# Optimization experiments

Hardware: AMD Instinct MI355X
Metric: run time of the kernel (lower is better)

The kernel has to match this reference:

```python
import jax, jax.numpy as jnp
import numpy as np

B, A, T, D = 8, 50, 256, 128
HEADS, C = 32, 4  # C = D // HEADS
NEG_SLOPE = 0.2   # PyG GATConv default negative_slope


def setup_inputs() -> dict:
    key = jax.random.key(0)
    k1, k2, k3, k4 = jax.random.split(key, 4)
    h = jax.random.normal(k1, (B, A, T, D), dtype=jnp.float32)
    # PyG Linear weight [heads*out, in], applied as x @ W.T
    W = jax.random.normal(k2, (HEADS * C, D), dtype=jnp.float32) * (1.0 / np.sqrt(D))
    att_src = jax.random.normal(k3, (HEADS, C), dtype=jnp.float32) * 0.1
    att_dst = jax.random.normal(k4, (HEADS, C), dtype=jnp.float32) * 0.1
    bias = jnp.zeros((HEADS * C,), dtype=jnp.float32)
    return {"h": h, "W": W, "att_src": att_src, "att_dst": att_dst, "bias": bias}


def reference(h, W, att_src, att_dst, bias):
    # Graph is fully-connected-minus-self over A agents, replicated B*T times.
    # Equivalent dense form: per-destination softmax over all sources j != i.
    Bv, Av, Tv, Dv = h.shape
    x = h.transpose(0, 2, 1, 3).reshape(Bv * Tv, Av, Dv)          # [N, A, D], N = B*T graphs
    x = jnp.einsum('nad,ed->nae', x, W).reshape(Bv * Tv, Av, HEADS, C)  # W x, per head
    a_src = jnp.einsum('nahc,hc->nah', x, att_src)                # alpha_src[j]
    a_dst = jnp.einsum('nahc,hc->nah', x, att_dst)                # alpha_dst[i]
    # edge (j -> i): e_ij = leaky_relu(alpha_src[j] + alpha_dst[i])
    e = a_dst[:, :, None, :] + a_src[:, None, :, :]               # [N, i, j, H]
    e = jnp.where(e > 0, e, NEG_SLOPE * e)
    diag = jnp.eye(Av, dtype=bool)[None, :, :, None]              # no self-loops
    e = jnp.where(diag, -jnp.inf, e)
    alpha = jax.nn.softmax(e, axis=2)                             # scatter-softmax over src per dst
    out = jnp.einsum('nijh,njhc->nihc', alpha, x)                 # scatter-add aggregation
    out = out.reshape(Bv * Tv, Av, HEADS * C) + bias              # concat heads + bias
    return out.reshape(Bv, Tv, Av, HEADS * C).transpose(0, 2, 1, 3)  # (B, A, T, D)
```

## Files before the change

kernel.cpp:

```cpp
#include <hip/hip_runtime.h>
#include <hip/hip_bf16.h>

#define LOG2E 1.4426950408889634f

typedef __attribute__((ext_vector_type(8))) short bf16x8;
typedef __attribute__((ext_vector_type(4))) float f32x4;
typedef __attribute__((ext_vector_type(2))) float v2f;

static __device__ __forceinline__ float fast_exp2(float x) {
    return __builtin_amdgcn_exp2f(x);
}
static __device__ __forceinline__ short bf16bits(float f) {
    __hip_bfloat16 b = __float2bfloat16(f);
    return *reinterpret_cast<short*>(&b);
}

__global__ void wconv(const float* __restrict__ W, short* __restrict__ Wb) {
    const int i = blockIdx.x * 256 + threadIdx.x;
    Wb[i] = bf16bits(W[i]);
}

template<bool PRE>
__global__ __launch_bounds__(256, 4) void gat_fused(
    const float* __restrict__ hsrc,
    const float* __restrict__ W,
    const short* __restrict__ Wb,
    const float* __restrict__ att_src,
    const float* __restrict__ att_dst,
    const float* __restrict__ bias,
    float* __restrict__ out)
{
    constexpr int A = 50, T = 256, D = 128, H = 32;
    __shared__ __align__(16) char smem[25600 + 12800];
    v2f*   EsFs = (v2f*)smem;
    v2f*   EdFd = (v2f*)(smem + 12800);
    short* hsb  = (short*)smem;
    short* xsb  = (short*)(smem + 25600);

    const int n = blockIdx.x;
    const int b = n >> 8;
    const int t = n & 255;
    const int tid = threadIdx.x;

    const float4* hg4 = (const float4*)hsrc;
    for (int idx = tid; idx < 64 * 32; idx += 256) {
        const int a = idx >> 5, k4 = idx & 31;
        short4 pk = {0, 0, 0, 0};
        if (a < A) {
            const float4 hv = hg4[((size_t)(b * A + a) * T + t) * 32 + k4];
            pk.x = bf16bits(hv.x); pk.y = bf16bits(hv.y);
            pk.z = bf16bits(hv.z); pk.w = bf16bits(hv.w);
        }
        const int swz = (k4 >> 1) ^ (a & 7);
        *(short4*)&hsb[a * 128 + swz * 8 + (k4 & 1) * 4] = pk;
    }
    __syncthreads();

    {
        const int wv = tid >> 6;
        const int lane = tid & 63;
        const int lr = lane & 15, lg = lane >> 4;
        const int n0 = wv * 32;
        f32x4 acc[4][2];
        #pragma unroll
        for (int m = 0; m < 4; ++m) {
            acc[m][0] = (f32x4){0.f, 0.f, 0.f, 0.f};
            acc[m][1] = (f32x4){0.f, 0.f, 0.f, 0.f};
        }
        #pragma unroll
        for (int kk = 0; kk < 4; ++kk) {
            bf16x8 bf0, bf1;
            if (PRE) {
                const bf16x8* Wb8 = (const bf16x8*)Wb;
                bf0 = Wb8[(size_t)(n0 + lr) * 16 + kk * 4 + lg];
                bf1 = Wb8[(size_t)(n0 + 16 + lr) * 16 + kk * 4 + lg];
            } else {
                const float4* W4 = (const float4*)W;
                const int kb = kk * 8 + lg * 2;
                const float4 wa = W4[(size_t)(n0 + lr) * 32 + kb];
                const float4 wb = W4[(size_t)(n0 + lr) * 32 + kb + 1];
                const float4 wc = W4[(size_t)(n0 + 16 + lr) * 32 + kb];
                const float4 wd = W4[(size_t)(n0 + 16 + lr) * 32 + kb + 1];
                bf0[0] = bf16bits(wa.x); bf0[1] = bf16bits(wa.y);
                bf0[2] = bf16bits(wa.z); bf0[3] = bf16bits(wa.w);
                bf0[4] = bf16bits(wb.x); bf0[5] = bf16bits(wb.y);
                bf0[6] = bf16bits(wb.z); bf0[7] = bf16bits(wb.w);
                bf1[0] = bf16bits(wc.x); bf1[1] = bf16bits(wc.y);
                bf1[2] = bf16bits(wc.z); bf1[3] = bf16bits(wc.w);
                bf1[4] = bf16bits(wd.x); bf1[5] = bf16bits(wd.y);
                bf1[6] = bf16bits(wd.z); bf1[7] = bf16bits(wd.w);
            }
            #pragma unroll
            for (int m = 0; m < 4; ++m) {
                const int row = m * 16 + lr;
                const int chunk = (kk * 4 + lg) ^ (row & 7);
                const bf16x8 af = *(const bf16x8*)&hsb[row * 128 + chunk * 8];
                acc[m][0] = __builtin_amdgcn_mfma_f32_16x16x32_bf16(af, bf0, acc[m][0], 0, 0, 0);
                acc[m][1] = __builtin_amdgcn_mfma_f32_16x16x32_bf16(af, bf1, acc[m][1], 0, 0, 0);
            }
        }
        #pragma unroll
        for (int m = 0; m < 4; ++m) {
            const int rb = m * 16 + lg * 4;
            #pragma unroll
            for (int nt = 0; nt < 2; ++nt) {
                const int col = n0 + nt * 16 + lr;
                #pragma unroll
                for (int r = 0; r < 4; ++r) {
                    if (rb + r < A) xsb[(rb + r) * D + col] = bf16bits(acc[m][nt][r]);
                }
            }
        }
    }
    __syncthreads();

    for (int idx = tid; idx < A * H; idx += 256) {
        const int hh = idx & 31, a = idx >> 5;
        const uint2 xq = *(const uint2*)&xsb[a * D + hh * 4];
        const float x0 = __uint_as_float(xq.x << 16);
        const float x1 = __uint_as_float(xq.x & 0xffff0000u);
        const float x2 = __uint_as_float(xq.y << 16);
        const float x3 = __uint_as_float(xq.y & 0xffff0000u);
        const float4 s4 = ((const float4*)att_src)[hh];
        const float4 d4 = ((const float4*)att_dst)[hh];
        const float asc = LOG2E * fmaf(x3, s4.w, fmaf(x2, s4.z, fmaf(x1, s4.y, x0 * s4.x)));
        const float ads = LOG2E * fmaf(x3, d4.w, fmaf(x2, d4.z, fmaf(x1, d4.y, x0 * d4.x)));
        EsFs[idx] = (v2f){fast_exp2(asc), fast_exp2(0.2f * asc)};
        EdFd[idx] = (v2f){fast_exp2(ads), fast_exp2(0.2f * ads)};
    }
    __syncthreads();

    {
        const int hh = tid & 31;
        const int ib = tid >> 5;
        v2f acc01[7], acc23[7], df[7];
        float l[7];
        #pragma unroll
        for (int r = 0; r < 7; ++r) {
            const int i = ib + 8 * r;
            const int ii = (i < A) ? i : (A - 1);
            df[r] = EdFd[ii * H + hh];
            acc01[r] = (v2f){0.f, 0.f};
            acc23[r] = (v2f){0.f, 0.f};
            l[r] = 0.f;
        }
        #pragma unroll 5
        for (int j = 0; j < A; ++j) {
            const v2f sf = EsFs[j * H + hh];
            const uint2 xq = *(const uint2*)&xsb[j * D + hh * 4];
            const v2f x01 = (v2f){__uint_as_float(xq.x << 16),
                                  __uint_as_float(xq.x & 0xffff0000u)};
            const v2f x23 = (v2f){__uint_as_float(xq.y << 16),
                                  __uint_as_float(xq.y & 0xffff0000u)};
            #pragma unroll
            for (int r = 0; r < 7; ++r) {
                const v2f pe = df[r] * sf;
                const float p = fmaxf(pe.x, pe.y);
                l[r] += p;
                const v2f pp = (v2f){p, p};
                acc01[r] = __builtin_elementwise_fma(pp, x01, acc01[r]);
                acc23[r] = __builtin_elementwise_fma(pp, x23, acc23[r]);
            }
        }
        const float4 bv = ((const float4*)bias)[hh];
        #pragma unroll
        for (int r = 0; r < 7; ++r) {
            const int i = ib + 8 * r;
            if (i < A) {
                const v2f sf = EsFs[i * H + hh];
                const uint2 xq = *(const uint2*)&xsb[i * D + hh * 4];
                const float xx0 = __uint_as_float(xq.x << 16);
                const float xx1 = __uint_as_float(xq.x & 0xffff0000u);
                const float xx2 = __uint_as_float(xq.y << 16);
                const float xx3 = __uint_as_float(xq.y & 0xffff0000u);
                const v2f pe = df[r] * sf;
                const float p = fmaxf(pe.x, pe.y);
                const float linv = 1.0f / (l[r] - p);
                float4 o;
                o.x = fmaf(acc01[r].x - p * xx0, linv, bv.x);
                o.y = fmaf(acc01[r].y - p * xx1, linv, bv.y);
                o.z = fmaf(acc23[r].x - p * xx2, linv, bv.z);
                o.w = fmaf(acc23[r].y - p * xx3, linv, bv.w);
                *(float4*)&out[((size_t)(b * A + i) * T + t) * D + hh * 4] = o;
            }
        }
    }
}

extern "C" void kernel_launch(void* const* d_in, const int* in_sizes, int n_in,
                              void* d_out, int out_size, void* d_ws, size_t ws_size,
                              hipStream_t stream) {
    const float* h       = (const float*)d_in[0];
    const float* W       = (const float*)d_in[1];
    const float* att_src = (const float*)d_in[2];
    const float* att_dst = (const float*)d_in[3];
    const float* bias    = (const float*)d_in[4];
    float* out = (float*)d_out;
    dim3 grid(8 * 256);
    dim3 block(256);
    if (ws_size >= 128 * 128 * sizeof(short)) {
        short* Wb = (short*)d_ws;
        hipLaunchKernelGGL(wconv, dim3(64), block, 0, stream, W, Wb);
        hipLaunchKernelGGL(gat_fused<true>, grid, block, 0, stream,
                           h, W, Wb, att_src, att_dst, bias, out);
    } else {
        hipLaunchKernelGGL(gat_fused<false>, grid, block, 0, stream,
                           h, W, (const short*)nullptr, att_src, att_dst, bias, out);
    }
}
```

Before: 59.99 us.

## Interleave projected features with source exp terms in shared memory and prefetch

Stores the bf16 head features and the source exp/exp-scaled terms side by side in one 16-byte record per (agent, head), overlaying the input staging buffer. The aggregation loop then does one 128-bit LDS load per source instead of two, and loads the next record a step ahead. This adds a barrier before the MFMA results are written, because the buffer is now reused. The shared-memory footprint changes a little, and the unroll drops from 5 to 2.

```diff
diff --git a/kernel.cpp b/kernel.cpp
--- a/kernel.cpp
+++ b/kernel.cpp
@@ -13,6 +13,9 @@
 static __device__ __forceinline__ short bf16bits(float f) {
     __hip_bfloat16 b = __float2bfloat16(f);
     return *reinterpret_cast<short*>(&b);
+}
+static __device__ __forceinline__ float bfbits2f(unsigned lo16) {
+    return __uint_as_float(lo16 << 16);
 }
 
 __global__ void wconv(const float* __restrict__ W, short* __restrict__ Wb) {
@@ -31,16 +34,17 @@
     float* __restrict__ out)
 {
     constexpr int A = 50, T = 256, D = 128, H = 32;
-    __shared__ __align__(16) char smem[25600 + 12800];
-    v2f*   EsFs = (v2f*)smem;
-    v2f*   EdFd = (v2f*)(smem + 12800);
+    __shared__ __align__(16) char smem[52 * 32 * 16 + A * H * 8];
+    char*  cxs  = smem;
+    v2f*   EdFd = (v2f*)(smem + 26624);
     short* hsb  = (short*)smem;
-    short* xsb  = (short*)(smem + 25600);
 
     const int n = blockIdx.x;
     const int b = n >> 8;
     const int t = n & 255;
     const int tid = threadIdx.x;
+    const int lane = tid & 63, lr = lane & 15, lg = lane >> 4;
+    const int wv = tid >> 6;
 
     const float4* hg4 = (const float4*)hsrc;
     for (int idx = tid; idx < 64 * 32; idx += 256) {
@@ -57,9 +61,6 @@
     __syncthreads();
 
     {
-        const int wv = tid >> 6;
-        const int lane = tid & 63;
-        const int lr = lane & 15, lg = lane >> 4;
         const int n0 = wv * 32;
         f32x4 acc[4][2];
         #pragma unroll
@@ -99,15 +100,18 @@
                 acc[m][1] = __builtin_amdgcn_mfma_f32_16x16x32_bf16(af, bf1, acc[m][1], 0, 0, 0);
             }
         }
+        __syncthreads();
         #pragma unroll
         for (int m = 0; m < 4; ++m) {
-            const int rb = m * 16 + lg * 4;
             #pragma unroll
             for (int nt = 0; nt < 2; ++nt) {
                 const int col = n0 + nt * 16 + lr;
+                const int boff = (col >> 2) * 16 + (col & 3) * 2;
                 #pragma unroll
                 for (int r = 0; r < 4; ++r) {
-                    if (rb + r < A) xsb[(rb + r) * D + col] = bf16bits(acc[m][nt][r]);
+                    const int row = m * 16 + lg * 4 + r;
+                    if (row < 52)
+                        *(short*)&cxs[row * 512 + boff] = bf16bits(acc[m][nt][r]);
                 }
             }
         }
@@ -115,17 +119,17 @@
     __syncthreads();
 
     for (int idx = tid; idx < A * H; idx += 256) {
-        const int hh = idx & 31, a = idx >> 5;
-        const uint2 xq = *(const uint2*)&xsb[a * D + hh * 4];
-        const float x0 = __uint_as_float(xq.x << 16);
+        const int hh = idx & 31;
+        const uint2 xq = *(const uint2*)&cxs[idx * 16];
+        const float x0 = bfbits2f(xq.x & 0xffffu);
         const float x1 = __uint_as_float(xq.x & 0xffff0000u);
-        const float x2 = __uint_as_float(xq.y << 16);
+        const float x2 = bfbits2f(xq.y & 0xffffu);
         const float x3 = __uint_as_float(xq.y & 0xffff0000u);
         const float4 s4 = ((const float4*)att_src)[hh];
         const float4 d4 = ((const float4*)att_dst)[hh];
         const float asc = LOG2E * fmaf(x3, s4.w, fmaf(x2, s4.z, fmaf(x1, s4.y, x0 * s4.x)));
         const float ads = LOG2E * fmaf(x3, d4.w, fmaf(x2, d4.z, fmaf(x1, d4.y, x0 * d4.x)));
-        EsFs[idx] = (v2f){fast_exp2(asc), fast_exp2(0.2f * asc)};
+        *(v2f*)&cxs[idx * 16 + 8] = (v2f){fast_exp2(asc), fast_exp2(0.2f * asc)};
         EdFd[idx] = (v2f){fast_exp2(ads), fast_exp2(0.2f * ads)};
     }
     __syncthreads();
@@ -144,14 +148,16 @@
             acc23[r] = (v2f){0.f, 0.f};
             l[r] = 0.f;
         }
-        #pragma unroll 5
+        const char* cp = &cxs[hh * 16];
+        uint4 cur = *(const uint4*)cp;
+        #pragma unroll 2
         for (int j = 0; j < A; ++j) {
-            const v2f sf = EsFs[j * H + hh];
-            const uint2 xq = *(const uint2*)&xsb[j * D + hh * 4];
-            const v2f x01 = (v2f){__uint_as_float(xq.x << 16),
-                                  __uint_as_float(xq.x & 0xffff0000u)};
-            const v2f x23 = (v2f){__uint_as_float(xq.y << 16),
-                                  __uint_as_float(xq.y & 0xffff0000u)};
+            const uint4 nxt = *(const uint4*)(cp + (j + 1) * 512);
+            const v2f sf = (v2f){__uint_as_float(cur.z), __uint_as_float(cur.w)};
+            const v2f x01 = (v2f){bfbits2f(cur.x & 0xffffu),
+                                  __uint_as_float(cur.x & 0xffff0000u)};
+            const v2f x23 = (v2f){bfbits2f(cur.y & 0xffffu),
+                                  __uint_as_float(cur.y & 0xffff0000u)};
             #pragma unroll
             for (int r = 0; r < 7; ++r) {
                 const v2f pe = df[r] * sf;
@@ -161,18 +167,19 @@
                 acc01[r] = __builtin_elementwise_fma(pp, x01, acc01[r]);
                 acc23[r] = __builtin_elementwise_fma(pp, x23, acc23[r]);
             }
+            cur = nxt;
         }
         const float4 bv = ((const float4*)bias)[hh];
         #pragma unroll
         for (int r = 0; r < 7; ++r) {
             const int i = ib + 8 * r;
             if (i < A) {
-                const v2f sf = EsFs[i * H + hh];
-                const uint2 xq = *(const uint2*)&xsb[i * D + hh * 4];
-                const float xx0 = __uint_as_float(xq.x << 16);
-                const float xx1 = __uint_as_float(xq.x & 0xffff0000u);
-                const float xx2 = __uint_as_float(xq.y << 16);
-                const float xx3 = __uint_as_float(xq.y & 0xffff0000u);
+                const uint4 ce = *(const uint4*)&cxs[(i * 32 + hh) * 16];
+                const v2f sf = (v2f){__uint_as_float(ce.z), __uint_as_float(ce.w)};
+                const float xx0 = bfbits2f(ce.x & 0xffffu);
+                const float xx1 = __uint_as_float(ce.x & 0xffff0000u);
+                const float xx2 = bfbits2f(ce.y & 0xffffu);
+                const float xx3 = __uint_as_float(ce.y & 0xffff0000u);
                 const v2f pe = df[r] * sf;
                 const float p = fmaxf(pe.x, pe.y);
                 const float linv = 1.0f / (l[r] - p);
```

Measured after the change: 59.54 us. About the same (-0.7%).
